# Optimization experiments

Measured on AMD Instinct MI355X. Metric: run time of the kernel, lower is better.

## Reference

```python
import jax, jax.numpy as jnp
import numpy as np

B, N, FIN = 64, 128, 768
NFEAT, NHID, NHEADS, NCLASS = 1024, 512, 8, 512
ALPHA = 0.2
NEG_E = -9e15
NEG_S = -9e10


def setup_inputs():
    rng = np.random.RandomState(0)
    x = rng.randn(B, N, FIN).astype(np.float32)
    offset_mapping = np.zeros((B, N, 2), dtype=np.int32)
    attention_mask = np.zeros((B, N), dtype=np.float32)
    tag = np.zeros((B, N), dtype=np.float32)
    for b in range(B):
        pos, k, groups = 1, 0, 0
        n_words = int(rng.randint(30, 60))
        for _ in range(n_words):
            wl = int(rng.randint(1, 4))
            if k + wl > 120:
                break
            for _t in range(wl):
                offset_mapping[b, k] = (pos, pos + 2)  # contiguous inside word
                pos += 2
                k += 1
            pos += 1  # 1-char gap => word boundary: end == next_start - 1
            groups += 1
        groups -= 1  # last word is never closed (matches torch loop semantics)
        attention_mask[b, :groups] = 1.0
        tag[b, :groups] = (rng.rand(groups) > 0.1).astype(np.float32)
        tag[b, 0] = 1.0
    adj = (rng.rand(B, N, N) < 0.3).astype(np.float32)
    adj = np.clip(adj + np.eye(N, dtype=np.float32)[None], 0.0, 1.0)
    s = 0.02
    p = {
        'Wg_w': s * rng.randn(FIN, NFEAT), 'Wg_b': np.zeros(NFEAT),
        'hW_w': s * rng.randn(NHEADS, NFEAT, NHID), 'hW_b': np.zeros((NHEADS, NHID)),
        'ha_w': s * rng.randn(NHEADS, 2 * NHID), 'ha_b': np.zeros(NHEADS),
        'oW_w': s * rng.randn(NHID * NHEADS, NCLASS), 'oW_b': np.zeros(NCLASS),
        'oa_w': s * rng.randn(2 * NCLASS), 'oa_b': np.zeros(()),
        'fin_w': s * rng.randn(NCLASS, 1), 'fin_b': np.zeros(1),
    }
    inp = {
        'x': jnp.asarray(x), 'tag': jnp.asarray(tag),
        'offset_mapping': jnp.asarray(offset_mapping),
        'attention_mask': jnp.asarray(attention_mask), 'adj': jnp.asarray(adj),
    }
    for kk, vv in p.items():
        inp[kk] = jnp.asarray(np.asarray(vv, dtype=np.float32))
    return inp


def _group_pool(x, offs):
    # Vectorized form of the offset-grouped mean pooling loop.
    zero = (offs[:, :, 0] == 0) & (offs[:, :, 1] == 0)  # padding rows
    fz = jnp.argmax(zero, axis=1)                       # first padding row (break)
    pos = jnp.arange(N)
    valid = pos[None, :] < fz[:, None]
    nxt_start = jnp.concatenate([offs[:, 1:, 0], jnp.zeros((offs.shape[0], 1), offs.dtype)], axis=1)
    boundary = valid & (offs[:, :, 1] == nxt_start - 1)
    bi = boundary.astype(jnp.int32)
    cs = jnp.cumsum(bi, axis=1)
    seg = cs - bi                 # exclusive cumsum: group id per token
    G = cs[:, -1]                 # number of closed groups per row

    def per(xb, segb, bb):
        sums = jax.ops.segment_sum(xb, segb, num_segments=N + 1)[:N]
        cnts = jax.ops.segment_sum(jnp.ones((N,), xb.dtype), segb, num_segments=N + 1)[:N]
        ends = jax.ops.segment_sum((jnp.arange(N) + 1) * bb, segb, num_segments=N + 1)[:N]
        return sums, cnts, ends

    sums, cnts, ends = jax.vmap(per)(x, seg, bi)
    g = jnp.arange(N)[None, :]
    gv = g < G[:, None]
    x_off = jnp.where(gv[..., None], sums / jnp.maximum(cnts, 1.0)[..., None], 0.0)
    starts = jnp.concatenate([jnp.zeros((offs.shape[0], 1), jnp.int32), ends[:, :-1]], axis=1)
    starts = jnp.where(gv, starts, 0)
    ends = jnp.where(gv, ends, 0)
    return x_off, jnp.stack([starts, ends], axis=-1)  # [B,N,F_in], [B,N,2]


def _expand_row(fix):
    # Flatten [start,end) ranges in order until the first [0,0] row; rest = arange.
    zr = (fix[:, 0] == 0) & (fix[:, 1] == 0)
    fz = jnp.argmax(zr)
    valid = jnp.arange(N) < fz
    lens = jnp.where(valid, fix[:, 1] - fix[:, 0], 0)
    csum = jnp.cumsum(lens)
    excl = csum - lens
    total = csum[-1]
    l = jnp.arange(N)
    k = jnp.clip(jnp.searchsorted(csum, l, side='right'), 0, N - 1)
    val = fix[k, 0] + (l - excl[k])
    return jnp.where(l < total, val, l)


def _scores(x_off, tag, attention_mask, adj, Wg_w, Wg_b, hW_w, hW_b, ha_w, ha_b, oW_w, oW_b, oa_w, oa_b, fin_w, fin_b):
    xw = x_off @ Wg_w + Wg_b                                    # [B,N,NFEAT]
    h = jnp.einsum('bnf,hfo->bhno', xw, hW_w) + hW_b[None, :, None, :]
    # e_ij = leakyrelu(a1.h_i + a2.h_j + b): decomposition of a([h_i||h_j])
    e = jax.nn.leaky_relu(
        jnp.einsum('bhno,ho->bhn', h, ha_w[:, :NHID])[:, :, :, None]
        + jnp.einsum('bhno,ho->bhn', h, ha_w[:, NHID:])[:, :, None, :]
        + ha_b[None, :, None, None], ALPHA)
    att = jax.nn.softmax(jnp.where(adj[:, None, :, :] > 0, e, NEG_E), axis=-1)
    x1 = jax.nn.elu(jnp.einsum('bhij,bhjo->bhio', att, h))
    x1 = x1.transpose(0, 2, 1, 3).reshape(x1.shape[0], N, NHEADS * NHID)
    h2 = x1 @ oW_w + oW_b
    e2 = jax.nn.leaky_relu((h2 @ oa_w[:NCLASS])[:, :, None]
                           + (h2 @ oa_w[NCLASS:])[:, None, :] + oa_b, ALPHA)
    att2 = jax.nn.softmax(jnp.where(adj > 0, e2, NEG_E), axis=-1)
    x2 = jax.nn.elu(jnp.einsum('bij,bjo->bio', att2, h2))
    logits = (x2 @ fin_w + fin_b)[..., 0]                        # [B,N]
    m = jnp.where(tag > 0, attention_mask, 0.0)
    sc = jax.nn.softmax(jnp.where(m > 0, logits * m, NEG_S), axis=1)
    summary = m.sum(axis=1)
    ii = (jnp.arange(N, 0, -1).astype(jnp.float32)[None, :] / summary[:, None]) * m
    ii = jax.nn.softmax(jnp.where(m > 0, ii, NEG_S), axis=1)
    return sc + ii


def reference(x, tag, offset_mapping, attention_mask, adj, Wg_w, Wg_b, hW_w, hW_b, ha_w, ha_b, oW_w, oW_b, oa_w, oa_b, fin_w, fin_b):
    x_off, index_group = _group_pool(x, offset_mapping)
    sc = _scores(x_off, tag, attention_mask, adj, Wg_w, Wg_b, hW_w, hW_b, ha_w, ha_b, oW_w, oW_b, oa_w, oa_b, fin_w, fin_b)
    order = jnp.argsort(-sc, axis=1)  # jax argsort is stable; matches torch stable descending
    bidx = jnp.arange(sc.shape[0])[:, None]
    fix = index_group.at[bidx, order].set(index_group)  # scatter_(dim=1) with permutation index
    return jax.vmap(_expand_row)(fix)
```

## Files before the change

### kernel.cpp

```cpp
#include <hip/hip_runtime.h>
#include <cstddef>
#include <cstdint>

#define B_ 64
#define N_ 128
#define FIN_ 768
#define NEG_E_ (-9.0e15f)
#define NEG_S_ (-9.0e10f)
#define CHUNK_ 16

typedef unsigned short u16;
typedef unsigned int u32;
typedef float f32x4 __attribute__((ext_vector_type(4)));
typedef short s16x8 __attribute__((ext_vector_type(8)));
typedef u16 u16x4 __attribute__((ext_vector_type(4)));
typedef u16 u16x2 __attribute__((ext_vector_type(2)));

__device__ __forceinline__ u16 f2bf(float x) {
  u32 u = __float_as_uint(x);
  return (u16)((u + 0x7fffu + ((u >> 16) & 1u)) >> 16);
}
__device__ __forceinline__ float b2f(u16 h) {
  return __uint_as_float(((u32)h) << 16);
}

__global__ __launch_bounds__(256) void group_pool_kernel(
    const float* __restrict__ x, const int* __restrict__ offs,
    u16* __restrict__ xoh, u16* __restrict__ xol, int* __restrict__ ig)
{
  const int b = blockIdx.x;
  const int fc = blockIdx.y;
  const int tid = threadIdx.x;
  __shared__ int o0[N_ + 1], o1[N_];
  __shared__ int bi[N_], cs[N_];
  __shared__ int st[N_], en[N_];
  __shared__ float invlen[N_];
  __shared__ int fzs;

  if (tid < N_) {
    o0[tid] = offs[(b * N_ + tid) * 2 + 0];
    o1[tid] = offs[(b * N_ + tid) * 2 + 1];
  }
  if (tid == 0) { o0[N_] = 0; fzs = N_; }
  __syncthreads();
  if (tid < N_ && o0[tid] == 0 && o1[tid] == 0) atomicMin(&fzs, tid);
  __syncthreads();
  const int fz = fzs;
  if (tid < N_) {
    int nxt = o0[tid + 1];
    bi[tid] = (tid < fz && o1[tid] == nxt - 1) ? 1 : 0;
    cs[tid] = bi[tid];
  }
  __syncthreads();
  for (int d = 1; d < N_; d <<= 1) {
    int v = 0;
    if (tid < N_ && tid >= d) v = cs[tid - d];
    __syncthreads();
    if (tid < N_) cs[tid] += v;
    __syncthreads();
  }
  if (tid < N_ && bi[tid]) en[cs[tid] - 1] = tid + 1;
  __syncthreads();
  const int G = cs[N_ - 1];
  if (tid < G) {
    int s = tid ? en[tid - 1] : 0;
    st[tid] = s;
    invlen[tid] = 1.0f / (float)(en[tid] - s);
  }
  __syncthreads();
  if (fc == 0 && tid < N_) {
    int g = tid;
    ig[(b * N_ + g) * 2 + 0] = (g < G) ? st[g] : 0;
    ig[(b * N_ + g) * 2 + 1] = (g < G) ? en[g] : 0;
  }

  const int f = fc * 128 + (tid & 63) * 2;
  const float* xb = x + (size_t)b * N_ * FIN_ + f;
  for (int g = tid >> 6; g < N_; g += 4) {
    u16 h0 = 0, h1 = 0, l0 = 0, l1 = 0;
    if (g < G) {
      int s = st[g], e = en[g];
      float s0 = 0.0f, s1 = 0.0f;
      for (int k = s; k < e; ++k) {
        float2 v = *(const float2*)(xb + (size_t)k * FIN_);
        s0 += v.x; s1 += v.y;
      }
      float il = invlen[g];
      float m0 = s0 * il, m1 = s1 * il;
      h0 = f2bf(m0); l0 = f2bf(m0 - b2f(h0));
      h1 = f2bf(m1); l1 = f2bf(m1 - b2f(h1));
    }
    size_t oo = ((size_t)b * N_ + g) * FIN_ + f;
    u16x2 hv = {h0, h1}, lv = {l0, l1};
    *(u16x2*)(xoh + oo) = hv;
    *(u16x2*)(xol + oo) = lv;
  }
}

__global__ __launch_bounds__(256) void pack_wgT(
    const float* __restrict__ w, u16* __restrict__ th, u16* __restrict__ tl)
{
  __shared__ float t[32][33];
  const int k0 = blockIdx.x * 32, n0 = blockIdx.y * 32;
  const int r = threadIdx.x >> 3;
  const int c = (threadIdx.x & 7) * 4;
  float4 v = *(const float4*)(w + (size_t)(k0 + r) * 1024 + n0 + c);
  t[r][c] = v.x; t[r][c + 1] = v.y; t[r][c + 2] = v.z; t[r][c + 3] = v.w;
  __syncthreads();
  u16x4 hv, lv;
#pragma unroll
  for (int i = 0; i < 4; ++i) {
    float xv = t[c + i][r];
    u16 h = f2bf(xv);
    hv[i] = h; lv[i] = f2bf(xv - b2f(h));
  }
  size_t dst = (size_t)(n0 + r) * 768 + k0 + c;
  *(u16x4*)(th + dst) = hv;
  *(u16x4*)(tl + dst) = lv;
}
__global__ __launch_bounds__(256) void pack_hwT(
    const float* __restrict__ w, u16* __restrict__ th, u16* __restrict__ tl)
{
  __shared__ float t[32][33];
  const int o0 = blockIdx.x * 32, f0 = blockIdx.y * 32, hd = blockIdx.z;
  const int r = threadIdx.x >> 3;
  const int c = (threadIdx.x & 7) * 4;
  float4 v = *(const float4*)(w + ((size_t)hd * 1024 + f0 + r) * 512 + o0 + c);
  t[r][c] = v.x; t[r][c + 1] = v.y; t[r][c + 2] = v.z; t[r][c + 3] = v.w;
  __syncthreads();
  u16x4 hv, lv;
#pragma unroll
  for (int i = 0; i < 4; ++i) {
    float xv = t[c + i][r];
    u16 h = f2bf(xv);
    hv[i] = h; lv[i] = f2bf(xv - b2f(h));
  }
  size_t dst = ((size_t)hd * 512 + o0 + r) * 1024 + f0 + c;
  *(u16x4*)(th + dst) = hv;
  *(u16x4*)(tl + dst) = lv;
}
__global__ __launch_bounds__(256) void pack_owT(
    const float* __restrict__ w, u16* __restrict__ th, u16* __restrict__ tl)
{
  __shared__ float t[32][33];
  const int k0 = blockIdx.x * 32, o0 = blockIdx.y * 32;
  const int r = threadIdx.x >> 3;
  const int c = (threadIdx.x & 7) * 4;
  float4 v = *(const float4*)(w + (size_t)(k0 + r) * 512 + o0 + c);
  t[r][c] = v.x; t[r][c + 1] = v.y; t[r][c + 2] = v.z; t[r][c + 3] = v.w;
  __syncthreads();
  u16x4 hv, lv;
#pragma unroll
  for (int i = 0; i < 4; ++i) {
    float xv = t[c + i][r];
    u16 h = f2bf(xv);
    hv[i] = h; lv[i] = f2bf(xv - b2f(h));
  }
  size_t dst = (size_t)(o0 + r) * 4096 + k0 + c;
  *(u16x4*)(th + dst) = hv;
  *(u16x4*)(tl + dst) = lv;
}

__global__ __launch_bounds__(256) void mfma_split_gemm(
    const u16* __restrict__ Ah, const u16* __restrict__ Al,
    const u16* __restrict__ Bh, const u16* __restrict__ Bl,
    const float* __restrict__ bias, int bias_mode,
    u16* __restrict__ Oh, u16* __restrict__ Ol, float* __restrict__ Of,
    int out_f32, int do_elu,
    int K, int lda, int ldb,
    long long Az, long long Bz,
    int msh, long long s_mb, int nsh, long long s_nb, long long s_n,
    long long zb_s, long long zh_s, int zH)
{
  __shared__ u16 As_h[128][40];
  __shared__ u16 As_l[128][40];
  __shared__ u16 Bs_h[128][40];
  __shared__ u16 Bs_l[128][40];
  const int tid = threadIdx.x;
  const int wave = tid >> 6, lane = tid & 63;
  const int wm = (wave >> 1) * 64, wn = (wave & 1) * 64;
  const int bn = blockIdx.x * 128, bm = blockIdx.y * 128;
  const int z = blockIdx.z;
  const u16* Ahb = Ah + (long long)z * Az;
  const u16* Alb = Al + (long long)z * Az;
  const u16* Bhb = Bh + (long long)z * Bz;
  const u16* Blb = Bl + (long long)z * Bz;
  const int lm = lane & 15, lq = lane >> 4;

  const int sr = tid >> 1;
  const int sc = (tid & 1) * 16;
  const size_t ga = (size_t)(bm + sr) * lda + sc;
  const size_t gb = (size_t)(bn + sr) * ldb + sc;

  f32x4 acc[4][4];
#pragma unroll
  for (int i = 0; i < 4; ++i)
#pragma unroll
    for (int j = 0; j < 4; ++j) acc[i][j] = (f32x4){0.0f, 0.0f, 0.0f, 0.0f};

  uint4 r0, r1, r2, r3, r4, r5, r6, r7;
  r0 = *(const uint4*)(Ahb + ga);
  r1 = *(const uint4*)(Ahb + ga + 8);
  r2 = *(const uint4*)(Alb + ga);
  r3 = *(const uint4*)(Alb + ga + 8);
  r4 = *(const uint4*)(Bhb + gb);
  r5 = *(const uint4*)(Bhb + gb + 8);
  r6 = *(const uint4*)(Blb + gb);
  r7 = *(const uint4*)(Blb + gb + 8);

  for (int k0 = 0; k0 < K; k0 += 32) {
    __syncthreads();
    *(uint4*)&As_h[sr][sc] = r0;
    *(uint4*)&As_h[sr][sc + 8] = r1;
    *(uint4*)&As_l[sr][sc] = r2;
    *(uint4*)&As_l[sr][sc + 8] = r3;
    *(uint4*)&Bs_h[sr][sc] = r4;
    *(uint4*)&Bs_h[sr][sc + 8] = r5;
    *(uint4*)&Bs_l[sr][sc] = r6;
    *(uint4*)&Bs_l[sr][sc + 8] = r7;
    __syncthreads();
    int kn = k0 + 32;
    if (kn < K) {
      r0 = *(const uint4*)(Ahb + ga + kn);
      r1 = *(const uint4*)(Ahb + ga + kn + 8);
      r2 = *(const uint4*)(Alb + ga + kn);
      r3 = *(const uint4*)(Alb + ga + kn + 8);
      r4 = *(const uint4*)(Bhb + gb + kn);
      r5 = *(const uint4*)(Bhb + gb + kn + 8);
      r6 = *(const uint4*)(Blb + gb + kn);
      r7 = *(const uint4*)(Blb + gb + kn + 8);
    }
    s16x8 fa_h[4], fa_l[4], fb_h[4], fb_l[4];
#pragma unroll
    for (int t = 0; t < 4; ++t) {
      fa_h[t] = *(const s16x8*)&As_h[wm + t * 16 + lm][lq * 8];
      fa_l[t] = *(const s16x8*)&As_l[wm + t * 16 + lm][lq * 8];
      fb_h[t] = *(const s16x8*)&Bs_h[wn + t * 16 + lm][lq * 8];
      fb_l[t] = *(const s16x8*)&Bs_l[wn + t * 16 + lm][lq * 8];
    }
#pragma unroll
    for (int i = 0; i < 4; ++i)
#pragma unroll
      for (int j = 0; j < 4; ++j) {
        acc[i][j] = __builtin_amdgcn_mfma_f32_16x16x32_bf16(fa_h[i], fb_h[j], acc[i][j], 0, 0, 0);
        acc[i][j] = __builtin_amdgcn_mfma_f32_16x16x32_bf16(fa_h[i], fb_l[j], acc[i][j], 0, 0, 0);
        acc[i][j] = __builtin_amdgcn_mfma_f32_16x16x32_bf16(fa_l[i], fb_h[j], acc[i][j], 0, 0, 0);
      }
  }

  __syncthreads();
  const long long zoff = (long long)(z / zH) * zb_s + (long long)(z % zH) * zh_s;
  const int mmask = (1 << msh) - 1;
  const int nmask = (1 << nsh) - 1;
  char* lds_raw = (char*)&As_h[0][0] + wave * 4608;
  const int rn = lane >> 2;
  const int rm = (lane & 3) * 16;

  if (out_f32) {
    float* slab = (float*)lds_raw;
#pragma unroll
    for (int j = 0; j < 4; ++j) {
#pragma unroll
      for (int i = 0; i < 4; ++i) {
        int mb = bm + wm + i * 16 + lq * 4;
        int n = bn + wn + j * 16 + lm;
        f32x4 v = acc[i][j];
        if (bias_mode == 1) v += bias[n];
        else if (bias_mode == 2) { f32x4 b4 = *(const f32x4*)&bias[mb]; v += b4; }
        if (do_elu) {
          v.x = v.x > 0.0f ? v.x : expm1f(v.x);
          v.y = v.y > 0.0f ? v.y : expm1f(v.y);
          v.z = v.z > 0.0f ? v.z : expm1f(v.z);
          v.w = v.w > 0.0f ? v.w : expm1f(v.w);
        }
        *(f32x4*)&slab[lm * 68 + i * 16 + lq * 4] = v;
      }
      __syncthreads();
      int n = bn + wn + j * 16 + rn;
      int mbase = bm + wm + rm;
      long long off = (long long)(mbase >> msh) * s_mb + (mbase & mmask)
                    + (long long)(n >> nsh) * s_nb + (long long)(n & nmask) * s_n + zoff;
      const float* src = &slab[rn * 68 + rm];
      f32x4 v0 = *(const f32x4*)(src + 0);
      f32x4 v1 = *(const f32x4*)(src + 4);
      f32x4 v2 = *(const f32x4*)(src + 8);
      f32x4 v3 = *(const f32x4*)(src + 12);
      *(f32x4*)(Of + off + 0)  = v0;
      *(f32x4*)(Of + off + 4)  = v1;
      *(f32x4*)(Of + off + 8)  = v2;
      *(f32x4*)(Of + off + 12) = v3;
      __syncthreads();
    }
  } else {
    u16* slab_h = (u16*)lds_raw;
    u16* slab_l = slab_h + 16 * 72;
#pragma unroll
    for (int j = 0; j < 4; ++j) {
#pragma unroll
      for (int i = 0; i < 4; ++i) {
        int mb = bm + wm + i * 16 + lq * 4;
        int n = bn + wn + j * 16 + lm;
        f32x4 v = acc[i][j];
        if (bias_mode == 1) v += bias[n];
        else if (bias_mode == 2) { f32x4 b4 = *(const f32x4*)&bias[mb]; v += b4; }
        if (do_elu) {
          v.x = v.x > 0.0f ? v.x : expm1f(v.x);
          v.y = v.y > 0.0f ? v.y : expm1f(v.y);
          v.z = v.z > 0.0f ? v.z : expm1f(v.z);
          v.w = v.w > 0.0f ? v.w : expm1f(v.w);
        }
        u16 h0 = f2bf(v.x), h1 = f2bf(v.y), h2 = f2bf(v.z), h3 = f2bf(v.w);
        u16x4 hv = {h0, h1, h2, h3};
        u16x4 lv = {f2bf(v.x - b2f(h0)), f2bf(v.y - b2f(h1)),
                    f2bf(v.z - b2f(h2)), f2bf(v.w - b2f(h3))};
        *(u16x4*)&slab_h[lm * 72 + i * 16 + lq * 4] = hv;
        *(u16x4*)&slab_l[lm * 72 + i * 16 + lq * 4] = lv;
      }
      __syncthreads();
      int n = bn + wn + j * 16 + rn;
      int mbase = bm + wm + rm;
      long long off = (long long)(mbase >> msh) * s_mb + (mbase & mmask)
                    + (long long)(n >> nsh) * s_nb + (long long)(n & nmask) * s_n + zoff;
      const u16* sh = &slab_h[rn * 72 + rm];
      const u16* sl = &slab_l[rn * 72 + rm];
      uint4 h0 = *(const uint4*)(sh + 0);
      uint4 h1 = *(const uint4*)(sh + 8);
      uint4 l0 = *(const uint4*)(sl + 0);
      uint4 l1 = *(const uint4*)(sl + 8);
      *(uint4*)(Oh + off + 0) = h0;
      *(uint4*)(Oh + off + 8) = h1;
      *(uint4*)(Ol + off + 0) = l0;
      *(uint4*)(Ol + off + 8) = l1;
      __syncthreads();
    }
  }
}

#define G8_BUF 49152

#define STAGE_A8(T) do { const int _t = (T); if (_t < nt) {                    \
    const int _q = _t % 3;                                                     \
    _Pragma("unroll")                                                          \
    for (int rg_ = 0; rg_ < 2; ++rg_)                                          \
      __builtin_amdgcn_global_load_lds(                                        \
          (const __attribute__((address_space(1))) void*)(gA +                 \
              (size_t)_t * 32 + (size_t)rg_ * 8 * lda),                        \
          (__attribute__((address_space(3))) void*)(ldsAd + _q * G8_BUF +      \
              rg_ * 1024),                                                     \
          16, 0, 0);                                                           \
  } } while (0)

#define STAGE_B8(T) do { const int _t = (T); if (_t < nt) {                    \
    const int _q = _t % 3;                                                     \
    _Pragma("unroll")                                                          \
    for (int rg_ = 0; rg_ < 4; ++rg_)                                          \
      __builtin_amdgcn_global_load_lds(                                        \
          (const __attribute__((address_space(1))) void*)(gB +                 \
              (size_t)_t * 32 + (size_t)rg_ * 8 * ldb),                        \
          (__attribute__((address_space(3))) void*)(ldsBd + _q * G8_BUF +      \
              rg_ * 1024),                                                     \
          16, 0, 0);                                                           \
  } } while (0)

__global__ __launch_bounds__(512, 2) void mfma_split_gemm8(
    const u16* __restrict__ Ah, const u16* __restrict__ Al,
    const u16* __restrict__ Bh, const u16* __restrict__ Bl,
    const float* __restrict__ bias, int bias_mode,
    u16* __restrict__ Oh, u16* __restrict__ Ol,
    float* __restrict__ Of, int out_f32,
    int K, int lda, int ldb,
    int msh, long long s_mb, int nsh, long long s_nb, long long s_n,
    int zKS, long long zOs)
{
  __shared__ __align__(128) char ldsb[3 * G8_BUF];
  const int tid = threadIdx.x;
  const int wave = tid >> 6, lane = tid & 63;
  const int wm = (wave >> 2) * 64, wn = (wave & 3) * 64;
  const int bn = blockIdx.x * 256, bm = blockIdx.y * 128;
  const int z = blockIdx.z;
  const int lm = lane & 15, lq = lane >> 4;
  const int nt = K >> 5;

  const int srow = lane >> 3;
  const int sl = (lane & 7) ^ srow;
  const int scol = (sl & 3) * 8;
  const u16* Asel = (sl < 4) ? Ah : Al;
  const u16* Bsel = (sl < 4) ? Bh : Bl;

  const u16* gA = Asel + (size_t)(bm + wave * 16 + srow) * lda + scol + (size_t)z * zKS;
  const u16* gB = Bsel + (size_t)(bn + wave * 32 + srow) * ldb + scol + (size_t)z * zKS;
  char* ldsAd = ldsb + wave * 2048;
  char* ldsBd = ldsb + 16384 + wave * 4096;

  const int hbyt = (lq ^ (lm & 7)) * 16;
  const int lbyt = hbyt ^ 64;

  f32x4 acc[4][4];
#pragma unroll
  for (int i = 0; i < 4; ++i)
#pragma unroll
    for (int j = 0; j < 4; ++j) acc[i][j] = (f32x4){0.0f, 0.0f, 0.0f, 0.0f};

  STAGE_A8(0); STAGE_B8(0);
  STAGE_A8(1); STAGE_B8(1);
  if (nt > 1) asm volatile("s_waitcnt vmcnt(6)" ::: "memory");
  else        asm volatile("s_waitcnt vmcnt(0)" ::: "memory");
  __builtin_amdgcn_s_barrier();
  __builtin_amdgcn_sched_barrier(0);

#pragma unroll 3
  for (int t = 0; t < nt; ++t) {
    const int q = t % 3;
    STAGE_A8(t + 2);
    STAGE_B8(t + 2);
    const char* Abase = ldsb + q * G8_BUF + (wm + lm) * 128;
    const char* Bbase = ldsb + q * G8_BUF + 16384 + (wn + lm) * 128;
    s16x8 fa[4][2], fb[4][2];
#pragma unroll
    for (int i = 0; i < 4; ++i) {
      fb[i][0] = *(const s16x8*)(Bbase + i * 2048 + hbyt);
      fb[i][1] = *(const s16x8*)(Bbase + i * 2048 + lbyt);
      fa[i][0] = *(const s16x8*)(Abase + i * 2048 + hbyt);
      fa[i][1] = *(const s16x8*)(Abase + i * 2048 + lbyt);
    }
    __builtin_amdgcn_s_setprio(1);
#pragma unroll
    for (int i = 0; i < 4; ++i)
#pragma unroll
      for (int j = 0; j < 4; ++j) {
        acc[i][j] = __builtin_amdgcn_mfma_f32_16x16x32_bf16(fa[i][0], fb[j][0], acc[i][j], 0, 0, 0);
        acc[i][j] = __builtin_amdgcn_mfma_f32_16x16x32_bf16(fa[i][0], fb[j][1], acc[i][j], 0, 0, 0);
        acc[i][j] = __builtin_amdgcn_mfma_f32_16x16x32_bf16(fa[i][1], fb[j][0], acc[i][j], 0, 0, 0);
      }
    __builtin_amdgcn_s_setprio(0);
    if (t + 1 < nt) {
      if (t + 2 < nt) asm volatile("s_waitcnt vmcnt(6)" ::: "memory");
      else            asm volatile("s_waitcnt vmcnt(0)" ::: "memory");
      __builtin_amdgcn_s_barrier();
      __builtin_amdgcn_sched_barrier(0);
    }
  }

  __syncthreads();
  const long long zoff = (long long)z * zOs;
  const int mmask = (1 << msh) - 1;
  const int nmask = (1 << nsh) - 1;
  char* lds_raw = ldsb + wave * 4608;
  const int rn = lane >> 2;
  const int rm = (lane & 3) * 16;

  if (out_f32) {
    float* slab = (float*)lds_raw;
#pragma unroll
    for (int j = 0; j < 4; ++j) {
#pragma unroll
      for (int i = 0; i < 4; ++i) {
        int mb = bm + wm + i * 16 + lq * 4;
        int n = bn + wn + j * 16 + lm;
        f32x4 v = acc[i][j];
        if (bias_mode == 1) v += bias[n];
        else if (bias_mode == 2) { f32x4 b4 = *(const f32x4*)&bias[mb]; v += b4; }
        *(f32x4*)&slab[lm * 68 + i * 16 + lq * 4] = v;
      }
      __syncthreads();
      int n = bn + wn + j * 16 + rn;
      int mbase = bm + wm + rm;
      long long off = (long long)(mbase >> msh) * s_mb + (mbase & mmask)
                    + (long long)(n >> nsh) * s_nb + (long long)(n & nmask) * s_n + zoff;
      const float* src = &slab[rn * 68 + rm];
      f32x4 v0 = *(const f32x4*)(src + 0);
      f32x4 v1 = *(const f32x4*)(src + 4);
      f32x4 v2 = *(const f32x4*)(src + 8);
      f32x4 v3 = *(const f32x4*)(src + 12);
      *(f32x4*)(Of + off + 0)  = v0;
      *(f32x4*)(Of + off + 4)  = v1;
      *(f32x4*)(Of + off + 8)  = v2;
      *(f32x4*)(Of + off + 12) = v3;
      __syncthreads();
    }
  } else {
    u16* slab_h = (u16*)lds_raw;
    u16* slab_l = slab_h + 16 * 72;
#pragma unroll
    for (int j = 0; j < 4; ++j) {
#pragma unroll
      for (int i = 0; i < 4; ++i) {
        int mb = bm + wm + i * 16 + lq * 4;
        int n = bn + wn + j * 16 + lm;
        f32x4 v = acc[i][j];
        if (bias_mode == 1) v += bias[n];
        else if (bias_mode == 2) { f32x4 b4 = *(const f32x4*)&bias[mb]; v += b4; }
        u16 h0 = f2bf(v.x), h1 = f2bf(v.y), h2 = f2bf(v.z), h3 = f2bf(v.w);
        u16x4 hv = {h0, h1, h2, h3};
        u16x4 lv = {f2bf(v.x - b2f(h0)), f2bf(v.y - b2f(h1)),
                    f2bf(v.z - b2f(h2)), f2bf(v.w - b2f(h3))};
        *(u16x4*)&slab_h[lm * 72 + i * 16 + lq * 4] = hv;
        *(u16x4*)&slab_l[lm * 72 + i * 16 + lq * 4] = lv;
      }
      __syncthreads();
      int n = bn + wn + j * 16 + rn;
      int mbase = bm + wm + rm;
      long long off = (long long)(mbase >> msh) * s_mb + (mbase & mmask)
                    + (long long)(n >> nsh) * s_nb + (long long)(n & nmask) * s_n + zoff;
      const u16* sh = &slab_h[rn * 72 + rm];
      const u16* slp = &slab_l[rn * 72 + rm];
      uint4 h0 = *(const uint4*)(sh + 0);
      uint4 h1 = *(const uint4*)(sh + 8);
      uint4 l0 = *(const uint4*)(slp + 0);
      uint4 l1 = *(const uint4*)(slp + 8);
      *(uint4*)(Oh + off + 0) = h0;
      *(uint4*)(Oh + off + 8) = h1;
      *(uint4*)(Ol + off + 0) = l0;
      *(uint4*)(Ol + off + 8) = l1;
      __syncthreads();
    }
  }
}

__global__ __launch_bounds__(256) void reduce8_bias(
    const float* __restrict__ ps, const float* __restrict__ bias,
    float* __restrict__ h2T, int col0)
{
  int base = (blockIdx.x * 256 + threadIdx.x) * 4;
  int o = base >> 11, m = base & 2047;
  f32x4 v = *(const f32x4*)(ps + base);
#pragma unroll
  for (int s = 1; s < 8; ++s)
    v += *(const f32x4*)(ps + base + (size_t)s * 1048576);
  v += bias[o];
  *(f32x4*)(h2T + (size_t)o * 8192 + col0 + m) = v;
}

__global__ __launch_bounds__(512) void fused_att1(
    const u16* __restrict__ hTh, const u16* __restrict__ hTl,
    const float* __restrict__ W,
    const float* __restrict__ hb,
    const float* __restrict__ adj,
    u16* __restrict__ atth, u16* __restrict__ attl)
{
  const int bh = blockIdx.x;
  const int head = bh & 7;
  const int bc = bh >> 3;
  const int tid = threadIdx.x;
  __shared__ float sh1[4][128], sh2[4][128];
  __shared__ float es[128], ed[128];

  {
    int os = tid >> 7, i = tid & 127;
    const u16* ph = hTh + (size_t)bh * 65536 + (size_t)os * 16384 + i;
    const u16* pl = hTl + (size_t)bh * 65536 + (size_t)os * 16384 + i;
    const float* w1 = W + head * 1024 + os * 128;
    float s1 = 0.0f, s2 = 0.0f;
#pragma unroll 8
    for (int o = 0; o < 128; ++o) {
      float hv = b2f(ph[o * 128]) + b2f(pl[o * 128]);
      s1 = fmaf(hv, w1[o], s1);
      s2 = fmaf(hv, w1[512 + o], s2);
    }
    sh1[os][i] = s1;
    sh2[os][i] = s2;
  }
  __syncthreads();
  if (tid < 128) {
    es[tid] = (sh1[0][tid] + sh1[1][tid] + sh1[2][tid] + sh1[3][tid]) + hb[head];
    ed[tid] = sh2[0][tid] + sh2[1][tid] + sh2[2][tid] + sh2[3][tid];
  }
  __syncthreads();

  const int w = tid >> 6, lane = tid & 63;
  const float* adjb = adj + (size_t)bc * 16384;
  for (int r = w * 16; r < w * 16 + 16; ++r) {
    float esr = es[r];
    float v0, v1;
    {
      float e = esr + ed[lane];
      e = (e >= 0.0f) ? e : 0.2f * e;
      v0 = (adjb[r * 128 + lane] > 0.0f) ? e : NEG_E_;
    }
    {
      float e = esr + ed[lane + 64];
      e = (e >= 0.0f) ? e : 0.2f * e;
      v1 = (adjb[r * 128 + lane + 64] > 0.0f) ? e : NEG_E_;
    }
    float mx = fmaxf(v0, v1);
    for (int off = 32; off; off >>= 1) mx = fmaxf(mx, __shfl_xor(mx, off));
    float e0 = expf(v0 - mx), e1 = expf(v1 - mx);
    float sm = e0 + e1;
    for (int off = 32; off; off >>= 1) sm += __shfl_xor(sm, off);
    float inv = 1.0f / sm;
    float p0 = e0 * inv, p1 = e1 * inv;
    size_t base = (size_t)(bh * 128 + r) * 128;
    u16 h0 = f2bf(p0), h1 = f2bf(p1);
    atth[base + lane] = h0;
    attl[base + lane] = f2bf(p0 - b2f(h0));
    atth[base + lane + 64] = h1;
    attl[base + lane + 64] = f2bf(p1 - b2f(h1));
  }
}

__global__ __launch_bounds__(512) void fused_att2(
    const float* __restrict__ h2T, const float* __restrict__ oa,
    const float* __restrict__ ob,
    const float* __restrict__ adj,
    float* __restrict__ attf)
{
  const int b = blockIdx.x;
  const int tid = threadIdx.x;
  __shared__ float sh1[4][128], sh2[4][128];
  __shared__ float es[128], ed[128];

  {
    int os = tid >> 7, i = tid & 127;
    const float* hp = h2T + (size_t)os * 128 * 8192 + b * 128 + i;
    const float* oa1 = oa + os * 128;
    float s1 = 0.0f, s2 = 0.0f;
#pragma unroll 8
    for (int o = 0; o < 128; ++o) {
      float hv = hp[(size_t)o * 8192];
      s1 = fmaf(hv, oa1[o], s1);
      s2 = fmaf(hv, oa1[512 + o], s2);
    }
    sh1[os][i] = s1;
    sh2[os][i] = s2;
  }
  __syncthreads();
  if (tid < 128) {
    es[tid] = (sh1[0][tid] + sh1[1][tid] + sh1[2][tid] + sh1[3][tid]) + ob[0];
    ed[tid] = sh2[0][tid] + sh2[1][tid] + sh2[2][tid] + sh2[3][tid];
  }
  __syncthreads();

  const int w = tid >> 6, lane = tid & 63;
  const float* adjb = adj + (size_t)b * 16384;
  for (int r = w * 16; r < w * 16 + 16; ++r) {
    float esr = es[r];
    float v0, v1;
    {
      float e = esr + ed[lane];
      e = (e >= 0.0f) ? e : 0.2f * e;
      v0 = (adjb[r * 128 + lane] > 0.0f) ? e : NEG_E_;
    }
    {
      float e = esr + ed[lane + 64];
      e = (e >= 0.0f) ? e : 0.2f * e;
      v1 = (adjb[r * 128 + lane + 64] > 0.0f) ? e : NEG_E_;
    }
    float mx = fmaxf(v0, v1);
    for (int off = 32; off; off >>= 1) mx = fmaxf(mx, __shfl_xor(mx, off));
    float e0 = expf(v0 - mx), e1 = expf(v1 - mx);
    float sm = e0 + e1;
    for (int off = 32; off; off >>= 1) sm += __shfl_xor(sm, off);
    float inv = 1.0f / sm;
    size_t base = (size_t)(b * 128 + r) * 128;
    attf[base + lane] = e0 * inv;
    attf[base + lane + 64] = e1 * inv;
  }
}

__global__ __launch_bounds__(256) void bgemm_elu_bt_f32(
    const float* __restrict__ A, const float* __restrict__ BT,
    float* __restrict__ C)
{
  __shared__ float As[16][64];
  __shared__ float Bs[16][68];
  const int tid = threadIdx.x;
  const int tm = blockIdx.x >> 3, tn = blockIdx.x & 7;
  const int bm = tm * 64, bn = tn * 64;
  const int b = blockIdx.y;
  const float* Ab = A + (size_t)b * 16384;
  const float* BTb = BT + (size_t)b * 128;
  const int ty = tid >> 4, tx = tid & 15;
  const int ar = tid >> 2, ac = (tid & 3) * 4;
  float acc[4][4];
#pragma unroll
  for (int i = 0; i < 4; ++i)
#pragma unroll
    for (int j = 0; j < 4; ++j) acc[i][j] = 0.0f;

  for (int k0 = 0; k0 < 128; k0 += 16) {
    float4 av = *(const float4*)(Ab + (size_t)(bm + ar) * 128 + k0 + ac);
    float4 bv = *(const float4*)(BTb + (size_t)(bn + ar) * 8192 + k0 + ac);
    __syncthreads();
    As[ac + 0][ar] = av.x; As[ac + 1][ar] = av.y; As[ac + 2][ar] = av.z; As[ac + 3][ar] = av.w;
    Bs[ac + 0][ar] = bv.x; Bs[ac + 1][ar] = bv.y; Bs[ac + 2][ar] = bv.z; Bs[ac + 3][ar] = bv.w;
    __syncthreads();
#pragma unroll
    for (int kk = 0; kk < 16; ++kk) {
      float a[4], bb[4];
      *(float4*)a  = *(const float4*)&As[kk][ty * 4];
      *(float4*)bb = *(const float4*)&Bs[kk][tx * 4];
#pragma unroll
      for (int i = 0; i < 4; ++i)
#pragma unroll
        for (int j = 0; j < 4; ++j)
          acc[i][j] = fmaf(a[i], bb[j], acc[i][j]);
    }
  }
#pragma unroll
  for (int i = 0; i < 4; ++i) {
    int row = b * 128 + bm + ty * 4 + i;
    float4 v;
    v.x = acc[i][0] > 0.0f ? acc[i][0] : expm1f(acc[i][0]);
    v.y = acc[i][1] > 0.0f ? acc[i][1] : expm1f(acc[i][1]);
    v.z = acc[i][2] > 0.0f ? acc[i][2] : expm1f(acc[i][2]);
    v.w = acc[i][3] > 0.0f ? acc[i][3] : expm1f(acc[i][3]);
    *(float4*)(C + (size_t)row * 512 + bn + tx * 4) = v;
  }
}

__global__ __launch_bounds__(256) void logits_kernel(
    const float* __restrict__ X, const float* __restrict__ w,
    const float* __restrict__ bptr, float* __restrict__ out, int R)
{
  int wv = (blockIdx.x * 256 + threadIdx.x) >> 6;
  int lane = threadIdx.x & 63;
  if (wv >= R) return;
  const float* xr = X + (size_t)wv * 512;
  float s = 0.0f;
#pragma unroll
  for (int i = 0; i < 8; ++i) {
    int c = lane + i * 64;
    s = fmaf(xr[c], w[c], s);
  }
  for (int off = 32; off; off >>= 1) s += __shfl_down(s, off);
  if (lane == 0) out[wv] = s + bptr[0];
}

__global__ __launch_bounds__(128) void finalize_kernel(
    const float* __restrict__ logits, const float* __restrict__ tag,
    const float* __restrict__ amask, const int* __restrict__ ig,
    int* __restrict__ out)
{
  const int b = blockIdx.x, tid = threadIdx.x;
  __shared__ float red[N_];
  __shared__ float scs[N_];
  __shared__ int fs[N_], fe[N_], lens[N_], csum[N_];
  __shared__ int redi[N_];

  float lg = logits[b * N_ + tid];
  float tg = tag[b * N_ + tid];
  float am = amask[b * N_ + tid];
  float m = (tg > 0.0f) ? am : 0.0f;

  float in1 = (m > 0.0f) ? lg * m : NEG_S_;
  red[tid] = in1; __syncthreads();
  for (int s = 64; s > 0; s >>= 1) { if (tid < s) red[tid] = fmaxf(red[tid], red[tid + s]); __syncthreads(); }
  float M1 = red[0]; __syncthreads();
  float e1 = expf(in1 - M1);
  red[tid] = e1; __syncthreads();
  for (int s = 64; s > 0; s >>= 1) { if (tid < s) red[tid] += red[tid + s]; __syncthreads(); }
  float S1 = red[0]; __syncthreads();
  float sc = e1 / S1;

  red[tid] = m; __syncthreads();
  for (int s = 64; s > 0; s >>= 1) { if (tid < s) red[tid] += red[tid + s]; __syncthreads(); }
  float SM = red[0]; __syncthreads();

  float in2 = (m > 0.0f) ? ((float)(N_ - tid) / SM) * m : NEG_S_;
  red[tid] = in2; __syncthreads();
  for (int s = 64; s > 0; s >>= 1) { if (tid < s) red[tid] = fmaxf(red[tid], red[tid + s]); __syncthreads(); }
  float M2 = red[0]; __syncthreads();
  float e2 = expf(in2 - M2);
  red[tid] = e2; __syncthreads();
  for (int s = 64; s > 0; s >>= 1) { if (tid < s) red[tid] += red[tid + s]; __syncthreads(); }
  float S2 = red[0]; __syncthreads();
  float ii = e2 / S2;

  scs[tid] = sc + ii;
  __syncthreads();

  float si = scs[tid];
  int rank = 0;
  for (int j = 0; j < N_; ++j) {
    float sj = scs[j];
    rank += (sj > si) || (sj == si && j < tid);
  }
  fs[tid] = ig[(b * N_ + rank) * 2 + 0];
  fe[tid] = ig[(b * N_ + rank) * 2 + 1];
  __syncthreads();

  redi[tid] = (fs[tid] == 0 && fe[tid] == 0) ? tid : N_;
  __syncthreads();
  for (int s = 64; s > 0; s >>= 1) { if (tid < s) redi[tid] = min(redi[tid], redi[tid + s]); __syncthreads(); }
  int fz = redi[0]; __syncthreads();
  lens[tid] = (tid < fz) ? (fe[tid] - fs[tid]) : 0;
  __syncthreads();
  if (tid == 0) {
    int r = 0;
    for (int k = 0; k < N_; ++k) { r += lens[k]; csum[k] = r; }
  }
  __syncthreads();
  int total = csum[N_ - 1];
  int l = tid;
  int k = 0;
  while (k < N_ && csum[k] <= l) ++k;
  if (k > N_ - 1) k = N_ - 1;
  int val = fs[k] + (l - (csum[k] - lens[k]));
  out[b * N_ + l] = (l < total) ? val : l;
}

extern "C" void kernel_launch(void* const* d_in, const int* in_sizes, int n_in,
                              void* d_out, int out_size, void* d_ws, size_t ws_size,
                              hipStream_t stream)
{
  const float* x     = (const float*)d_in[0];
  const float* tag   = (const float*)d_in[1];
  const int*   offs  = (const int*)  d_in[2];
  const float* amask = (const float*)d_in[3];
  const float* adj   = (const float*)d_in[4];
  const float* Wg_w  = (const float*)d_in[5];
  const float* Wg_b  = (const float*)d_in[6];
  const float* hW_w  = (const float*)d_in[7];
  const float* hW_b  = (const float*)d_in[8];
  const float* ha_w  = (const float*)d_in[9];
  const float* ha_b  = (const float*)d_in[10];
  const float* oW_w  = (const float*)d_in[11];
  const float* oW_b  = (const float*)d_in[12];
  const float* oa_w  = (const float*)d_in[13];
  const float* oa_b  = (const float*)d_in[14];
  const float* fin_w = (const float*)d_in[15];
  const float* fin_b = (const float*)d_in[16];
  int* out = (int*)d_out;

  char* ws = (char*)d_ws;
  size_t o = 0;
  int* ig     = (int*)(ws + o);  o += 131072;
  u16* WgT_h  = (u16*)(ws + o);  o += 1572864;
  u16* WgT_l  = (u16*)(ws + o);  o += 1572864;
  u16* hWT_h  = (u16*)(ws + o);  o += 8388608;
  u16* hWT_l  = (u16*)(ws + o);  o += 8388608;
  u16* oWT_h  = (u16*)(ws + o);  o += 4194304;
  u16* oWT_l  = (u16*)(ws + o);  o += 4194304;
  float* h2T  = (float*)(ws + o); o += 16777216;
  o += 196608;
  float* lgts = (float*)(ws + o); o += 32768;
  u16* xw_h   = (u16*)(ws + o);  o += 16777216;
  u16* xw_l   = (u16*)(ws + o);  o += 16777216;
  char* pool  = ws + o;          o += 75497472;

  u16* xoff_h = (u16*)(pool + 0);
  u16* xoff_l = (u16*)(pool + 12582912);
  u16* hT_h   = (u16*)(pool + 0);
  u16* hT_l   = (u16*)(pool + 16777216);
  u16* x1_h   = (u16*)(pool + 33554432);
  u16* x1_l   = (u16*)(pool + 50331648);
  u16* att_h  = (u16*)(pool + 67108864);
  u16* att_l  = (u16*)(pool + 71303168);
  float* ps   = (float*)(pool + 0);
  float* att2 = (float*)(pool + 0);
  float* x2   = (float*)(pool + 4194304);

  pack_wgT<<<dim3(24, 32), 256, 0, stream>>>(Wg_w, WgT_h, WgT_l);
  pack_hwT<<<dim3(16, 32, 8), 256, 0, stream>>>(hW_w, hWT_h, hWT_l);
  pack_owT<<<dim3(128, 16), 256, 0, stream>>>(oW_w, oWT_h, oWT_l);

  group_pool_kernel<<<dim3(B_, 6), 256, 0, stream>>>(x, offs, xoff_h, xoff_l, ig);

  mfma_split_gemm8<<<dim3(32, 8, 1), 512, 0, stream>>>(
      WgT_h, WgT_l, xoff_h, xoff_l, Wg_b, 2,
      xw_h, xw_l, nullptr, 0,
      768, 768, 768,
      10, 0, 13, 0, 1024, 0, 0);

  for (int b0 = 0; b0 < B_; b0 += CHUNK_) {
    mfma_split_gemm8<<<dim3(16, 16, 1), 512, 0, stream>>>(
        xw_h + (size_t)b0 * 131072, xw_l + (size_t)b0 * 131072,
        hWT_h, hWT_l, hW_b, 1,
        hT_h, hT_l, nullptr, 0,
        1024, 1024, 1024,
        7, 524288, 9, 65536, 128, 0, 0);

    fused_att1<<<CHUNK_ * 8, 512, 0, stream>>>(
        hT_h, hT_l, ha_w, ha_b, adj + (size_t)b0 * 16384, att_h, att_l);

    mfma_split_gemm<<<dim3(1, 4, CHUNK_ * 8), 256, 0, stream>>>(
        hT_h, hT_l, att_h, att_l, nullptr, 0,
        x1_h, x1_l, nullptr, 0, 1,
        128, 128, 128, 65536, 16384,
        9, 0, 7, 0, 4096, 524288, 512, 8);

    mfma_split_gemm8<<<dim3(2, 16, 8), 512, 0, stream>>>(
        x1_h, x1_l, oWT_h, oWT_l, nullptr, 0,
        nullptr, nullptr, ps, 1,
        512, 4096, 4096,
        13, 0, 9, 0, 2048, 512, 1048576);
    reduce8_bias<<<1024, 256, 0, stream>>>(ps, oW_b, h2T, b0 * 128);
  }

  fused_att2<<<64, 512, 0, stream>>>(h2T, oa_w, oa_b, adj, att2);
  bgemm_elu_bt_f32<<<dim3(16, 64), 256, 0, stream>>>(att2, h2T, x2);

  logits_kernel<<<2048, 256, 0, stream>>>(x2, fin_w, fin_b, lgts, 8192);
  finalize_kernel<<<B_, 128, 0, stream>>>(lgts, tag, amask, ig, out);
}
```

Baseline: 817.7 us.

## Replace generic split GEMM for att@h with specialized x1 kernel

Swaps the generic split-bf16 MFMA GEMM used for the per-head attention x hidden product with a dedicated kernel. The whole 128x128 attention matrix for a (batch, head) is staged once in LDS, and each wave reads its hidden-state A fragments straight from global memory, so there is no per-k-tile double-buffered LDS staging or the barriers that came with it. The grid changes from 4 blocks of 256 threads to 2 blocks of 512 threads per (batch, head). The ELU and hi/lo bf16 split epilogue is rewritten with a per-wave LDS transpose, writing the hi and lo outputs in two passes. The cost is that ELU is computed twice, and the direct global fragment loads may be less coalesced.

```diff
diff --git a/kernel.cpp b/kernel.cpp
--- a/kernel.cpp
+++ b/kernel.cpp
@@ -161,178 +161,124 @@
   *(u16x4*)(tl + dst) = lv;
 }
 
-__global__ __launch_bounds__(256) void mfma_split_gemm(
-    const u16* __restrict__ Ah, const u16* __restrict__ Al,
-    const u16* __restrict__ Bh, const u16* __restrict__ Bl,
-    const float* __restrict__ bias, int bias_mode,
-    u16* __restrict__ Oh, u16* __restrict__ Ol, float* __restrict__ Of,
-    int out_f32, int do_elu,
-    int K, int lda, int ldb,
-    long long Az, long long Bz,
-    int msh, long long s_mb, int nsh, long long s_nb, long long s_n,
-    long long zb_s, long long zh_s, int zH)
-{
-  __shared__ u16 As_h[128][40];
-  __shared__ u16 As_l[128][40];
-  __shared__ u16 Bs_h[128][40];
-  __shared__ u16 Bs_l[128][40];
+__global__ __launch_bounds__(512, 1) void x1t_kernel(
+    const u16* __restrict__ hTh, const u16* __restrict__ hTl,
+    const u16* __restrict__ atth, const u16* __restrict__ attl,
+    u16* __restrict__ x1h, u16* __restrict__ x1l)
+{
+  __shared__ __align__(16) u16 lds[40960];
+  u16* Bs_h = lds;
+  u16* Bs_l = lds + 17408;
   const int tid = threadIdx.x;
   const int wave = tid >> 6, lane = tid & 63;
-  const int wm = (wave >> 1) * 64, wn = (wave & 1) * 64;
-  const int bn = blockIdx.x * 128, bm = blockIdx.y * 128;
-  const int z = blockIdx.z;
-  const u16* Ahb = Ah + (long long)z * Az;
-  const u16* Alb = Al + (long long)z * Az;
-  const u16* Bhb = Bh + (long long)z * Bz;
-  const u16* Blb = Bl + (long long)z * Bz;
   const int lm = lane & 15, lq = lane >> 4;
-
-  const int sr = tid >> 1;
-  const int sc = (tid & 1) * 16;
-  const size_t ga = (size_t)(bm + sr) * lda + sc;
-  const size_t gb = (size_t)(bn + sr) * ldb + sc;
-
-  f32x4 acc[4][4];
-#pragma unroll
-  for (int i = 0; i < 4; ++i)
-#pragma unroll
-    for (int j = 0; j < 4; ++j) acc[i][j] = (f32x4){0.0f, 0.0f, 0.0f, 0.0f};
-
-  uint4 r0, r1, r2, r3, r4, r5, r6, r7;
-  r0 = *(const uint4*)(Ahb + ga);
-  r1 = *(const uint4*)(Ahb + ga + 8);
-  r2 = *(const uint4*)(Alb + ga);
-  r3 = *(const uint4*)(Alb + ga + 8);
-  r4 = *(const uint4*)(Bhb + gb);
-  r5 = *(const uint4*)(Bhb + gb + 8);
-  r6 = *(const uint4*)(Blb + gb);
-  r7 = *(const uint4*)(Blb + gb + 8);
-
-  for (int k0 = 0; k0 < K; k0 += 32) {
-    __syncthreads();
-    *(uint4*)&As_h[sr][sc] = r0;
-    *(uint4*)&As_h[sr][sc + 8] = r1;
-    *(uint4*)&As_l[sr][sc] = r2;
-    *(uint4*)&As_l[sr][sc + 8] = r3;
-    *(uint4*)&Bs_h[sr][sc] = r4;
-    *(uint4*)&Bs_h[sr][sc + 8] = r5;
-    *(uint4*)&Bs_l[sr][sc] = r6;
-    *(uint4*)&Bs_l[sr][sc + 8] = r7;
-    __syncthreads();
-    int kn = k0 + 32;
-    if (kn < K) {
-      r0 = *(const uint4*)(Ahb + ga + kn);
-      r1 = *(const uint4*)(Ahb + ga + kn + 8);
-      r2 = *(const uint4*)(Alb + ga + kn);
-      r3 = *(const uint4*)(Alb + ga + kn + 8);
-      r4 = *(const uint4*)(Bhb + gb + kn);
-      r5 = *(const uint4*)(Bhb + gb + kn + 8);
-      r6 = *(const uint4*)(Blb + gb + kn);
-      r7 = *(const uint4*)(Blb + gb + kn + 8);
-    }
-    s16x8 fa_h[4], fa_l[4], fb_h[4], fb_l[4];
-#pragma unroll
-    for (int t = 0; t < 4; ++t) {
-      fa_h[t] = *(const s16x8*)&As_h[wm + t * 16 + lm][lq * 8];
-      fa_l[t] = *(const s16x8*)&As_l[wm + t * 16 + lm][lq * 8];
-      fb_h[t] = *(const s16x8*)&Bs_h[wn + t * 16 + lm][lq * 8];
-      fb_l[t] = *(const s16x8*)&Bs_l[wn + t * 16 + lm][lq * 8];
-    }
-#pragma unroll
-    for (int i = 0; i < 4; ++i)
-#pragma unroll
-      for (int j = 0; j < 4; ++j) {
-        acc[i][j] = __builtin_amdgcn_mfma_f32_16x16x32_bf16(fa_h[i], fb_h[j], acc[i][j], 0, 0, 0);
-        acc[i][j] = __builtin_amdgcn_mfma_f32_16x16x32_bf16(fa_h[i], fb_l[j], acc[i][j], 0, 0, 0);
-        acc[i][j] = __builtin_amdgcn_mfma_f32_16x16x32_bf16(fa_l[i], fb_h[j], acc[i][j], 0, 0, 0);
+  const int mhalf = blockIdx.x;
+  const int z = blockIdx.y;
+  const int mbase = mhalf * 256 + wave * 32;
+
+  {
+    const u16* az_h = atth + (size_t)z * 16384;
+    const u16* az_l = attl + (size_t)z * 16384;
+#pragma unroll
+    for (int p = 0; p < 4; ++p) {
+      int row = p * 32 + (tid >> 4);
+      int s16 = tid & 15;
+      uint4 vh = *(const uint4*)(az_h + row * 128 + s16 * 8);
+      uint4 vl = *(const uint4*)(az_l + row * 128 + s16 * 8);
+      *(uint4*)&Bs_h[row * 136 + s16 * 8] = vh;
+      *(uint4*)&Bs_l[row * 136 + s16 * 8] = vl;
+    }
+  }
+  const u16* gAh = hTh + (size_t)z * 65536 + (size_t)mbase * 128;
+  const u16* gAl = hTl + (size_t)z * 65536 + (size_t)mbase * 128;
+  __syncthreads();
+
+  f32x4 acc[2][8];
+#pragma unroll
+  for (int t = 0; t < 2; ++t)
+#pragma unroll
+    for (int n = 0; n < 8; ++n) acc[t][n] = (f32x4){0.0f, 0.0f, 0.0f, 0.0f};
+
+#pragma unroll
+  for (int kk = 0; kk < 4; ++kk) {
+    s16x8 fa_h[2], fa_l[2];
+#pragma unroll
+    for (int t = 0; t < 2; ++t) {
+      size_t ao = (size_t)(t * 16 + lm) * 128 + kk * 32 + lq * 8;
+      fa_h[t] = *(const s16x8*)(gAh + ao);
+      fa_l[t] = *(const s16x8*)(gAl + ao);
+    }
+#pragma unroll
+    for (int nf = 0; nf < 8; ++nf) {
+      int boff = (nf * 16 + lm) * 136 + (kk * 4 + lq) * 8;
+      s16x8 fb_h = *(const s16x8*)&Bs_h[boff];
+      s16x8 fb_l = *(const s16x8*)&Bs_l[boff];
+#pragma unroll
+      for (int t = 0; t < 2; ++t) {
+        acc[t][nf] = __builtin_amdgcn_mfma_f32_16x16x32_bf16(fa_h[t], fb_h, acc[t][nf], 0, 0, 0);
+        acc[t][nf] = __builtin_amdgcn_mfma_f32_16x16x32_bf16(fa_h[t], fb_l, acc[t][nf], 0, 0, 0);
+        acc[t][nf] = __builtin_amdgcn_mfma_f32_16x16x32_bf16(fa_l[t], fb_h, acc[t][nf], 0, 0, 0);
       }
-  }
-
-  __syncthreads();
-  const long long zoff = (long long)(z / zH) * zb_s + (long long)(z % zH) * zh_s;
-  const int mmask = (1 << msh) - 1;
-  const int nmask = (1 << nsh) - 1;
-  char* lds_raw = (char*)&As_h[0][0] + wave * 4608;
-  const int rn = lane >> 2;
-  const int rm = (lane & 3) * 16;
-
-  if (out_f32) {
-    float* slab = (float*)lds_raw;
-#pragma unroll
-    for (int j = 0; j < 4; ++j) {
-#pragma unroll
-      for (int i = 0; i < 4; ++i) {
-        int mb = bm + wm + i * 16 + lq * 4;
-        int n = bn + wn + j * 16 + lm;
-        f32x4 v = acc[i][j];
-        if (bias_mode == 1) v += bias[n];
-        else if (bias_mode == 2) { f32x4 b4 = *(const f32x4*)&bias[mb]; v += b4; }
-        if (do_elu) {
-          v.x = v.x > 0.0f ? v.x : expm1f(v.x);
-          v.y = v.y > 0.0f ? v.y : expm1f(v.y);
-          v.z = v.z > 0.0f ? v.z : expm1f(v.z);
-          v.w = v.w > 0.0f ? v.w : expm1f(v.w);
-        }
-        *(f32x4*)&slab[lm * 68 + i * 16 + lq * 4] = v;
-      }
-      __syncthreads();
-      int n = bn + wn + j * 16 + rn;
-      int mbase = bm + wm + rm;
-      long long off = (long long)(mbase >> msh) * s_mb + (mbase & mmask)
-                    + (long long)(n >> nsh) * s_nb + (long long)(n & nmask) * s_n + zoff;
-      const float* src = &slab[rn * 68 + rm];
-      f32x4 v0 = *(const f32x4*)(src + 0);
-      f32x4 v1 = *(const f32x4*)(src + 4);
-      f32x4 v2 = *(const f32x4*)(src + 8);
-      f32x4 v3 = *(const f32x4*)(src + 12);
-      *(f32x4*)(Of + off + 0)  = v0;
-      *(f32x4*)(Of + off + 4)  = v1;
-      *(f32x4*)(Of + off + 8)  = v2;
-      *(f32x4*)(Of + off + 12) = v3;
-      __syncthreads();
-    }
-  } else {
-    u16* slab_h = (u16*)lds_raw;
-    u16* slab_l = slab_h + 16 * 72;
-#pragma unroll
-    for (int j = 0; j < 4; ++j) {
-#pragma unroll
-      for (int i = 0; i < 4; ++i) {
-        int mb = bm + wm + i * 16 + lq * 4;
-        int n = bn + wn + j * 16 + lm;
-        f32x4 v = acc[i][j];
-        if (bias_mode == 1) v += bias[n];
-        else if (bias_mode == 2) { f32x4 b4 = *(const f32x4*)&bias[mb]; v += b4; }
-        if (do_elu) {
-          v.x = v.x > 0.0f ? v.x : expm1f(v.x);
-          v.y = v.y > 0.0f ? v.y : expm1f(v.y);
-          v.z = v.z > 0.0f ? v.z : expm1f(v.z);
-          v.w = v.w > 0.0f ? v.w : expm1f(v.w);
-        }
-        u16 h0 = f2bf(v.x), h1 = f2bf(v.y), h2 = f2bf(v.z), h3 = f2bf(v.w);
-        u16x4 hv = {h0, h1, h2, h3};
-        u16x4 lv = {f2bf(v.x - b2f(h0)), f2bf(v.y - b2f(h1)),
-                    f2bf(v.z - b2f(h2)), f2bf(v.w - b2f(h3))};
-        *(u16x4*)&slab_h[lm * 72 + i * 16 + lq * 4] = hv;
-        *(u16x4*)&slab_l[lm * 72 + i * 16 + lq * 4] = lv;
-      }
-      __syncthreads();
-      int n = bn + wn + j * 16 + rn;
-      int mbase = bm + wm + rm;
-      long long off = (long long)(mbase >> msh) * s_mb + (mbase & mmask)
-                    + (long long)(n >> nsh) * s_nb + (long long)(n & nmask) * s_n + zoff;
-      const u16* sh = &slab_h[rn * 72 + rm];
-      const u16* sl = &slab_l[rn * 72 + rm];
-      uint4 h0 = *(const uint4*)(sh + 0);
-      uint4 h1 = *(const uint4*)(sh + 8);
-      uint4 l0 = *(const uint4*)(sl + 0);
-      uint4 l1 = *(const uint4*)(sl + 8);
-      *(uint4*)(Oh + off + 0) = h0;
-      *(uint4*)(Oh + off + 8) = h1;
-      *(uint4*)(Ol + off + 0) = l0;
-      *(uint4*)(Ol + off + 8) = l1;
-      __syncthreads();
-    }
+    }
+  }
+
+  __syncthreads();
+
+  u16* slab = lds + wave * 5120;
+  const size_t outb = (size_t)(z >> 3) * 524288 + (size_t)(z & 7) * 512 + mbase;
+#pragma unroll
+  for (int nf = 0; nf < 8; ++nf)
+#pragma unroll
+    for (int t = 0; t < 2; ++t) {
+      f32x4 v = acc[t][nf];
+      v.x = v.x > 0.0f ? v.x : expm1f(v.x);
+      v.y = v.y > 0.0f ? v.y : expm1f(v.y);
+      v.z = v.z > 0.0f ? v.z : expm1f(v.z);
+      v.w = v.w > 0.0f ? v.w : expm1f(v.w);
+      u16x4 hv = {f2bf(v.x), f2bf(v.y), f2bf(v.z), f2bf(v.w)};
+      *(u16x4*)&slab[(nf * 16 + lm) * 40 + t * 16 + lq * 4] = hv;
+    }
+#pragma unroll
+  for (int vv = 0; vv < 2; ++vv) {
+    int nn = lane + vv * 64;
+    const u16* sr = &slab[nn * 40];
+    u16* dst = x1h + outb + (size_t)nn * 4096;
+    uint4 a0 = *(const uint4*)(sr + 0);
+    uint4 a1 = *(const uint4*)(sr + 8);
+    uint4 a2 = *(const uint4*)(sr + 16);
+    uint4 a3 = *(const uint4*)(sr + 24);
+    *(uint4*)(dst + 0)  = a0;
+    *(uint4*)(dst + 8)  = a1;
+    *(uint4*)(dst + 16) = a2;
+    *(uint4*)(dst + 24) = a3;
+  }
+#pragma unroll
+  for (int nf = 0; nf < 8; ++nf)
+#pragma unroll
+    for (int t = 0; t < 2; ++t) {
+      f32x4 v = acc[t][nf];
+      v.x = v.x > 0.0f ? v.x : expm1f(v.x);
+      v.y = v.y > 0.0f ? v.y : expm1f(v.y);
+      v.z = v.z > 0.0f ? v.z : expm1f(v.z);
+      v.w = v.w > 0.0f ? v.w : expm1f(v.w);
+      u16 h0 = f2bf(v.x), h1 = f2bf(v.y), h2 = f2bf(v.z), h3 = f2bf(v.w);
+      u16x4 lv = {f2bf(v.x - b2f(h0)), f2bf(v.y - b2f(h1)),
+                  f2bf(v.z - b2f(h2)), f2bf(v.w - b2f(h3))};
+      *(u16x4*)&slab[(nf * 16 + lm) * 40 + t * 16 + lq * 4] = lv;
+    }
+#pragma unroll
+  for (int vv = 0; vv < 2; ++vv) {
+    int nn = lane + vv * 64;
+    const u16* sr = &slab[nn * 40];
+    u16* dst = x1l + outb + (size_t)nn * 4096;
+    uint4 a0 = *(const uint4*)(sr + 0);
+    uint4 a1 = *(const uint4*)(sr + 8);
+    uint4 a2 = *(const uint4*)(sr + 16);
+    uint4 a3 = *(const uint4*)(sr + 24);
+    *(uint4*)(dst + 0)  = a0;
+    *(uint4*)(dst + 8)  = a1;
+    *(uint4*)(dst + 16) = a2;
+    *(uint4*)(dst + 24) = a3;
   }
 }
 
@@ -873,11 +819,8 @@
     fused_att1<<<CHUNK_ * 8, 512, 0, stream>>>(
         hT_h, hT_l, ha_w, ha_b, adj + (size_t)b0 * 16384, att_h, att_l);
 
-    mfma_split_gemm<<<dim3(1, 4, CHUNK_ * 8), 256, 0, stream>>>(
-        hT_h, hT_l, att_h, att_l, nullptr, 0,
-        x1_h, x1_l, nullptr, 0, 1,
-        128, 128, 128, 65536, 16384,
-        9, 0, 7, 0, 4096, 524288, 512, 8);
+    x1t_kernel<<<dim3(2, CHUNK_ * 8), 512, 0, stream>>>(
+        hT_h, hT_l, att_h, att_l, x1_h, x1_l);
 
     mfma_split_gemm8<<<dim3(2, 16, 8), 512, 0, stream>>>(
         x1_h, x1_l, oWT_h, oWT_l, nullptr, 0,
```

Result: no change. 831.7 us (+1.7%).
